# Kernel tuning notes

Measured on AMD Instinct MI355X. Metric: run time of the kernel, lower is better.

## Reference

```python
import jax, jax.numpy as jnp
import numpy as np

VOCAB = 50257
EMBED = 1024


def setup_inputs() -> dict:
    key = jax.random.key(0)
    ks = jax.random.split(key, 8)
    s = 1.0 / np.sqrt(EMBED)  # PyTorch LSTM init scale (for realistic magnitudes)
    return {
        "input": jax.random.randint(ks[0], (1,), 0, VOCAB, dtype=jnp.int64),
        "hidden_state": jax.random.normal(ks[1], (1, 1, EMBED), dtype=jnp.float32),
        "cell_state": jax.random.normal(ks[2], (1, 1, EMBED), dtype=jnp.float32),
        "embed_table": jax.random.normal(ks[3], (VOCAB, EMBED), dtype=jnp.float32),
        "W_ih": jax.random.normal(ks[4], (4 * EMBED, EMBED), dtype=jnp.float32) * s,
        "W_hh": jax.random.normal(ks[5], (4 * EMBED, EMBED), dtype=jnp.float32) * s,
        "b_ih": jax.random.normal(ks[6], (4 * EMBED,), dtype=jnp.float32) * s,
        "b_hh": jax.random.normal(ks[7], (4 * EMBED,), dtype=jnp.float32) * s,
    }


def reference(input, hidden_state, cell_state, embed_table, W_ih, W_hh, b_ih, b_hh):
    # Embedding lookup: token id -> [EMBED]
    x = embed_table[input[0]]                      # [E]
    h = hidden_state[0, 0]                         # [E]
    c = cell_state[0, 0]                           # [E]
    # Single LSTM step, PyTorch gate order: i, f, g, o
    gates = W_ih @ x + b_ih + W_hh @ h + b_hh      # [4E]
    i, f, g, o = jnp.split(gates, 4)
    i = jax.nn.sigmoid(i)
    f = jax.nn.sigmoid(f)
    g = jnp.tanh(g)
    o = jax.nn.sigmoid(o)
    c_new = f * c + i * g
    h_new = o * jnp.tanh(c_new)
    return (h_new.reshape(1, 1, EMBED), c_new.reshape(1, 1, EMBED))
```

## Files before the change

### kernel.cpp

```cpp
#include <hip/hip_runtime.h>
#include <math.h>

#define EMBED 1024

typedef float f32x4 __attribute__((ext_vector_type(4)));

__device__ __forceinline__ float dot4(f32x4 a, f32x4 b) {
    return a[0] * b[0] + a[1] * b[1] + a[2] * b[2] + a[3] * b[3];
}

__global__ __launch_bounds__(512) void lstm_step_kernel(
    const unsigned int* __restrict__ tok,
    const float* __restrict__ h_in,
    const float* __restrict__ c_in,
    const float* __restrict__ embed,
    const float* __restrict__ W_ih,
    const float* __restrict__ W_hh,
    const float* __restrict__ b_ih,
    const float* __restrict__ b_hh,
    float* __restrict__ out)
{
    __shared__ float part[8];

    const int tid  = threadIdx.x;
    const int j    = blockIdx.x;
    const int w    = tid >> 6;
    const int lane = tid & 63;
    const int gate = w >> 1;
    const int half = w & 1;
    const int row  = gate * EMBED + j;

    const float* Wm = half ? W_hh : W_ih;
    const f32x4* wr = (const f32x4*)(Wm + (size_t)row * EMBED);
    f32x4 a0 = __builtin_nontemporal_load(wr + lane);
    f32x4 a1 = __builtin_nontemporal_load(wr + lane + 64);
    f32x4 a2 = __builtin_nontemporal_load(wr + lane + 128);
    f32x4 a3 = __builtin_nontemporal_load(wr + lane + 192);

    const float bias  = half ? b_hh[row] : b_ih[row];
    const float c_val = (w == 0) ? c_in[j] : 0.f;

    const float* vbase;
    if (half) {
        vbase = h_in;
    } else {
        const unsigned int t = tok[0];
        vbase = embed + (size_t)t * EMBED;
    }
    const f32x4* v4 = (const f32x4*)vbase;
    f32x4 b0 = v4[lane];
    f32x4 b1 = v4[lane + 64];
    f32x4 b2 = v4[lane + 128];
    f32x4 b3 = v4[lane + 192];

    float acc = dot4(a0, b0) + dot4(a1, b1) + dot4(a2, b2) + dot4(a3, b3);

    #pragma unroll
    for (int off = 32; off > 0; off >>= 1)
        acc += __shfl_xor(acc, off);

    if (lane == 0)
        part[w] = acc + bias;
    __syncthreads();

    if (tid == 0) {
        const float gi = part[0] + part[1];
        const float gf = part[2] + part[3];
        const float gg = part[4] + part[5];
        const float go = part[6] + part[7];
        const float i = 1.f / (1.f + __expf(-gi));
        const float f = 1.f / (1.f + __expf(-gf));
        const float e2g = __expf(2.f * gg);
        const float g = (e2g - 1.f) / (e2g + 1.f);
        const float o = 1.f / (1.f + __expf(-go));
        const float c_new = f * c_val + i * g;
        const float e2c = __expf(2.f * c_new);
        const float tc  = (e2c - 1.f) / (e2c + 1.f);
        out[j]         = o * tc;
        out[EMBED + j] = c_new;
    }
}

extern "C" void kernel_launch(void* const* d_in, const int* in_sizes, int n_in,
                              void* d_out, int out_size, void* d_ws, size_t ws_size,
                              hipStream_t stream) {
    const unsigned int* tok  = (const unsigned int*)d_in[0];
    const float* h_in  = (const float*)d_in[1];
    const float* c_in  = (const float*)d_in[2];
    const float* embed = (const float*)d_in[3];
    const float* W_ih  = (const float*)d_in[4];
    const float* W_hh  = (const float*)d_in[5];
    const float* b_ih  = (const float*)d_in[6];
    const float* b_hh  = (const float*)d_in[7];
    float* out = (float*)d_out;

    lstm_step_kernel<<<EMBED, 512, 0, stream>>>(
        tok, h_in, c_in, embed, W_ih, W_hh, b_ih, b_hh, out);
}
```

Measured before the change: 9.774 us.

## Process two hidden units per block with each wave covering both weight matrices

Each block now handles two output units instead of one, and each wave computes a full gate row across both W_ih and W_hh. This halves the grid size, lets every wave load both the x and h vectors, and gives each wave twice as many in-flight weight loads. The cost is more register pressure and fewer blocks to spread across the GPU's compute units.

```diff
diff --git a/kernel.cpp b/kernel.cpp
--- a/kernel.cpp
+++ b/kernel.cpp
@@ -23,37 +23,40 @@
     __shared__ float part[8];
 
     const int tid  = threadIdx.x;
-    const int j    = blockIdx.x;
     const int w    = tid >> 6;
     const int lane = tid & 63;
-    const int gate = w >> 1;
-    const int half = w & 1;
+    const int jj   = w >> 2;
+    const int gate = w & 3;
+    const int j    = (blockIdx.x << 1) + jj;
     const int row  = gate * EMBED + j;
 
-    const float* Wm = half ? W_hh : W_ih;
-    const f32x4* wr = (const f32x4*)(Wm + (size_t)row * EMBED);
-    f32x4 a0 = __builtin_nontemporal_load(wr + lane);
-    f32x4 a1 = __builtin_nontemporal_load(wr + lane + 64);
-    f32x4 a2 = __builtin_nontemporal_load(wr + lane + 128);
-    f32x4 a3 = __builtin_nontemporal_load(wr + lane + 192);
+    const f32x4* wi = (const f32x4*)(W_ih + (size_t)row * EMBED);
+    const f32x4* wh = (const f32x4*)(W_hh + (size_t)row * EMBED);
+    f32x4 a0 = __builtin_nontemporal_load(wi + lane);
+    f32x4 a1 = __builtin_nontemporal_load(wi + lane + 64);
+    f32x4 a2 = __builtin_nontemporal_load(wi + lane + 128);
+    f32x4 a3 = __builtin_nontemporal_load(wi + lane + 192);
+    f32x4 c0 = __builtin_nontemporal_load(wh + lane);
+    f32x4 c1 = __builtin_nontemporal_load(wh + lane + 64);
+    f32x4 c2 = __builtin_nontemporal_load(wh + lane + 128);
+    f32x4 c3 = __builtin_nontemporal_load(wh + lane + 192);
 
-    const float bias  = half ? b_hh[row] : b_ih[row];
-    const float c_val = (w == 0) ? c_in[j] : 0.f;
+    const float bias = b_ih[row] + b_hh[row];
 
-    const float* vbase;
-    if (half) {
-        vbase = h_in;
-    } else {
-        const unsigned int t = tok[0];
-        vbase = embed + (size_t)t * EMBED;
-    }
-    const f32x4* v4 = (const f32x4*)vbase;
-    f32x4 b0 = v4[lane];
-    f32x4 b1 = v4[lane + 64];
-    f32x4 b2 = v4[lane + 128];
-    f32x4 b3 = v4[lane + 192];
+    const unsigned int t = tok[0];
+    const f32x4* x4 = (const f32x4*)(embed + (size_t)t * EMBED);
+    const f32x4* h4 = (const f32x4*)h_in;
+    f32x4 x0 = x4[lane];
+    f32x4 x1 = x4[lane + 64];
+    f32x4 x2 = x4[lane + 128];
+    f32x4 x3 = x4[lane + 192];
+    f32x4 h0 = h4[lane];
+    f32x4 h1 = h4[lane + 64];
+    f32x4 h2 = h4[lane + 128];
+    f32x4 h3 = h4[lane + 192];
 
-    float acc = dot4(a0, b0) + dot4(a1, b1) + dot4(a2, b2) + dot4(a3, b3);
+    float acc = dot4(a0, x0) + dot4(a1, x1) + dot4(a2, x2) + dot4(a3, x3)
+              + dot4(c0, h0) + dot4(c1, h1) + dot4(c2, h2) + dot4(c3, h3);
 
     #pragma unroll
     for (int off = 32; off > 0; off >>= 1)
@@ -63,21 +66,23 @@
         part[w] = acc + bias;
     __syncthreads();
 
-    if (tid == 0) {
-        const float gi = part[0] + part[1];
-        const float gf = part[2] + part[3];
-        const float gg = part[4] + part[5];
-        const float go = part[6] + part[7];
+    if ((tid & 255) == 0) {
+        const int base = (tid >> 6);
+        const int jm   = (blockIdx.x << 1) + (tid >> 8);
+        const float gi = part[base + 0];
+        const float gf = part[base + 1];
+        const float gg = part[base + 2];
+        const float go = part[base + 3];
         const float i = 1.f / (1.f + __expf(-gi));
         const float f = 1.f / (1.f + __expf(-gf));
         const float e2g = __expf(2.f * gg);
         const float g = (e2g - 1.f) / (e2g + 1.f);
         const float o = 1.f / (1.f + __expf(-go));
-        const float c_new = f * c_val + i * g;
+        const float c_new = f * c_in[jm] + i * g;
         const float e2c = __expf(2.f * c_new);
         const float tc  = (e2c - 1.f) / (e2c + 1.f);
-        out[j]         = o * tc;
-        out[EMBED + j] = c_new;
+        out[jm]         = o * tc;
+        out[EMBED + jm] = c_new;
     }
 }
 
@@ -94,6 +99,6 @@
     const float* b_hh  = (const float*)d_in[7];
     float* out = (float*)d_out;
 
-    lstm_step_kernel<<<EMBED, 512, 0, stream>>>(
+    lstm_step_kernel<<<EMBED / 2, 512, 0, stream>>>(
         tok, h_in, c_in, embed, W_ih, W_hh, b_ih, b_hh, out);
 }
```

Result: no change. 9.878 us (+1.1%).
